# Kernel tuning notes

Measured on AMD Instinct MI355X. Metric: run time of the kernel, lower is better.

The kernel has to match this reference:

```python
import jax, jax.numpy as jnp
import numpy as np

B, S, HID = 2, 2048, 1024
NH, HD = 16, 64
EPS = 1e-12


def setup_inputs() -> dict:
    key = jax.random.key(0)
    ks = jax.random.split(key, 6)
    w_scale = 1.0 / np.sqrt(HID)
    return {
        "hidden_states": jax.random.normal(ks[0], (B, S, HID), dtype=jnp.float32),
        "attention_mask": jnp.ones((B, S), dtype=jnp.float32),
        "Wq": jax.random.normal(ks[1], (HID, HID), dtype=jnp.float32) * w_scale,
        "bq": jnp.zeros((HID,), dtype=jnp.float32),
        "Wk": jax.random.normal(ks[2], (HID, HID), dtype=jnp.float32) * w_scale,
        "bk": jnp.zeros((HID,), dtype=jnp.float32),
        "Wv": jax.random.normal(ks[3], (HID, HID), dtype=jnp.float32) * w_scale,
        "bv": jnp.zeros((HID,), dtype=jnp.float32),
        "Wd": jax.random.normal(ks[4], (HID, HID), dtype=jnp.float32) * w_scale,
        "bd": jnp.zeros((HID,), dtype=jnp.float32),
        "ln_gamma": jnp.ones((HID,), dtype=jnp.float32),
        "ln_beta": jnp.zeros((HID,), dtype=jnp.float32),
    }


def _heads(x):  # [B,S,HID] -> [B,NH,S,HD]
    return x.reshape(B, S, NH, HD).transpose(0, 2, 1, 3)


def reference(hidden_states, attention_mask, Wq, bq, Wk, bk, Wv, bv, Wd, bd, ln_gamma, ln_beta):
    # pre-LayerNorm
    mu = jnp.mean(hidden_states, axis=-1, keepdims=True)
    var = jnp.mean(jnp.square(hidden_states - mu), axis=-1, keepdims=True)
    h = (hidden_states - mu) * jax.lax.rsqrt(var + EPS) * ln_gamma + ln_beta

    q = _heads(h @ Wq.T + bq)  # [B,NH,S,HD]
    k = _heads(h @ Wk.T + bk)
    v = _heads(h @ Wv.T + bv)

    # additive mask: -1000 * (1 - mask), broadcast over heads and query pos
    add_mask = -1000.0 * (1.0 - attention_mask)[:, None, None, :]  # [B,1,1,S]

    # scale applied symmetrically to q and k: sqrt(sqrt(HD)) each
    scale = np.sqrt(np.sqrt(HD)).astype(np.float32)
    scores = jnp.einsum("bhqd,bhkd->bhqk", q / scale, k / scale) + add_mask
    probs = jax.nn.softmax(scores, axis=-1)  # dropout p=0 -> identity
    ctx = jnp.einsum("bhqk,bhkd->bhqd", probs, v)  # [B,NH,S,HD]

    ctx = ctx.transpose(0, 2, 1, 3).reshape(B, S, HID)
    return ctx @ Wd.T + bd
```

## Files before the change

### kernel.cpp

```cpp
#include <hip/hip_runtime.h>
#include <hip/hip_bf16.h>
#include <math.h>

#define BATCH 2
#define SEQ   2048
#define HID   1024
#define NH    16
#define HD    64
#define MROWS (BATCH * SEQ)
#define VSTR  4160

typedef unsigned short u16;
typedef short bf16x8 __attribute__((ext_vector_type(8)));
typedef short bf16x4 __attribute__((ext_vector_type(4)));
typedef float f32x4  __attribute__((ext_vector_type(4)));

#define LOG2E 1.4426950408889634f
#define C2    (0.125f * LOG2E)
#define M2F   23.083120f

static __device__ __forceinline__ u16 f2bf(float f) {
    union { float f; unsigned int u; } v; v.f = f;
    unsigned int r = (v.u + 0x7FFF + ((v.u >> 16) & 1)) >> 16;
    return (u16)r;
}

static __device__ __forceinline__ unsigned int pk_bf16(float a, float b) {
    union { __hip_bfloat162 h; unsigned int u; } r;
    float2 f; f.x = a; f.y = b;
    r.h = __float22bfloat162_rn(f);
    return r.u;
}

static __device__ __forceinline__ f32x4 mfma16(bf16x8 a, bf16x8 b, f32x4 c) {
    return __builtin_amdgcn_mfma_f32_16x16x32_bf16(a, b, c, 0, 0, 0);
}

static __device__ __forceinline__ f32x4 mfma16k16(bf16x4 a, bf16x4 b, f32x4 c) {
#if __has_builtin(__builtin_amdgcn_mfma_f32_16x16x16bf16_1k)
    return __builtin_amdgcn_mfma_f32_16x16x16bf16_1k(a, b, c, 0, 0, 0);
#else
    bf16x8 a8 = {a[0], a[1], a[2], a[3], 0, 0, 0, 0};
    bf16x8 b8 = {b[0], b[1], b[2], b[3], 0, 0, 0, 0};
    return __builtin_amdgcn_mfma_f32_16x16x32_bf16(a8, b8, c, 0, 0, 0);
#endif
}

static __device__ __forceinline__ void ldsload16(const void* g, void* l) {
    __builtin_amdgcn_global_load_lds(
        (const __attribute__((address_space(1))) void*)(unsigned long long)(uintptr_t)g,
        (__attribute__((address_space(3))) void*)(unsigned int)(uintptr_t)l,
        16, 0, 0);
}

__global__ __launch_bounds__(256) void prep_kernel(const float* __restrict__ x,
                                                   const float* __restrict__ gamma,
                                                   const float* __restrict__ beta,
                                                   u16* __restrict__ h,
                                                   const float* __restrict__ w0,
                                                   const float* __restrict__ w1,
                                                   const float* __restrict__ w2,
                                                   const float* __restrict__ w3,
                                                   u16* o0, u16* o1, u16* o2, u16* o3,
                                                   const float* __restrict__ maskg,
                                                   float* __restrict__ m2g)
{
    __shared__ float red[8];
    const int t = threadIdx.x;
    if (blockIdx.x >= 8192) {
        const int idx = ((blockIdx.x - 8192) * 256 + t) * 4;
        const float4 m = *(const float4*)(maskg + idx);
        float4 o;
        o.x = fmaf(-1000.0f * (1.0f - m.x), LOG2E, -M2F);
        o.y = fmaf(-1000.0f * (1.0f - m.y), LOG2E, -M2F);
        o.z = fmaf(-1000.0f * (1.0f - m.z), LOG2E, -M2F);
        o.w = fmaf(-1000.0f * (1.0f - m.w), LOG2E, -M2F);
        *(float4*)(m2g + idx) = o;
        return;
    }
    if (blockIdx.x < 4096) {
        const int blk = blockIdx.x;
        const int which = blk >> 10;
        const int lb = blk & 1023;
        const float* src = which == 0 ? w0 : which == 1 ? w1 : which == 2 ? w2 : w3;
        u16* dst = which == 0 ? o0 : which == 1 ? o1 : which == 2 ? o2 : o3;
        const int idx = (lb * 256 + t) * 4;
        const float4 f = *(const float4*)(src + idx);
        union { u16 s[4]; uint2 v; } p;
        p.s[0] = f2bf(f.x); p.s[1] = f2bf(f.y); p.s[2] = f2bf(f.z); p.s[3] = f2bf(f.w);
        *(uint2*)(dst + idx) = p.v;
        return;
    }
    const int row = blockIdx.x - 4096;
    const float4 xv = ((const float4*)(x + (size_t)row * HID))[t];
    float s  = xv.x + xv.y + xv.z + xv.w;
    float ss = xv.x * xv.x + xv.y * xv.y + xv.z * xv.z + xv.w * xv.w;
#pragma unroll
    for (int off = 32; off > 0; off >>= 1) {
        s  += __shfl_down(s, off);
        ss += __shfl_down(ss, off);
    }
    const int wid = t >> 6;
    if ((t & 63) == 0) { red[wid] = s; red[4 + wid] = ss; }
    __syncthreads();
    s  = red[0] + red[1] + red[2] + red[3];
    ss = red[4] + red[5] + red[6] + red[7];
    const float mu   = s * (1.0f / HID);
    const float var  = ss * (1.0f / HID) - mu * mu;
    const float rstd = rsqrtf(var + 1e-12f);
    const float4 g  = ((const float4*)gamma)[t];
    const float4 bb = ((const float4*)beta)[t];
    union { u16 s[4]; uint2 v; } p;
    p.s[0] = f2bf((xv.x - mu) * rstd * g.x + bb.x);
    p.s[1] = f2bf((xv.y - mu) * rstd * g.y + bb.y);
    p.s[2] = f2bf((xv.z - mu) * rstd * g.z + bb.z);
    p.s[3] = f2bf((xv.w - mu) * rstd * g.w + bb.w);
    ((uint2*)(h + (size_t)row * HID))[t] = p.v;
}

static __device__ __forceinline__ void gemm_core(const u16* __restrict__ A,
                                                 const u16* __restrict__ B,
                                                 int K, int bm, int bn,
                                                 u16* As, u16* Bs,
                                                 int wave, int lane,
                                                 f32x4 acc[4][4])
{
    const int l15  = lane & 15;
    const int quad = lane >> 4;
    const int wm = (wave >> 1) * 64;
    const int wn = (wave & 1) * 64;

    const int c1 = wave * 64 + lane;
    const int c2 = c1 + 256;
    const u16* A1 = A + (size_t)(bm + (c1 >> 2)) * K + (c1 & 3) * 8;
    const u16* A2 = A + (size_t)(bm + (c2 >> 2)) * K + (c2 & 3) * 8;
    const u16* B1 = B + (size_t)(bn + (c1 >> 2)) * K + (c1 & 3) * 8;
    const u16* B2 = B + (size_t)(bn + (c2 >> 2)) * K + (c2 & 3) * 8;
    const int o1 = wave * 512;
    const int o2 = 2048 + wave * 512;

    ldsload16(A1, As + o1);
    ldsload16(A2, As + o2);
    ldsload16(B1, Bs + o1);
    ldsload16(B2, Bs + o2);

    const int nstep = K >> 5;
    for (int i = 0; i < nstep; i++) {
        __syncthreads();
        const int cb = (i & 1) * 4096;
        if (i + 1 < nstep) {
            const int nb = ((i + 1) & 1) * 4096;
            const int k0 = (i + 1) * 32;
            ldsload16(A1 + k0, As + nb + o1);
            ldsload16(A2 + k0, As + nb + o2);
            ldsload16(B1 + k0, Bs + nb + o1);
            ldsload16(B2 + k0, Bs + nb + o2);
        }
        bf16x8 af[4], bfr[4];
#pragma unroll
        for (int mt = 0; mt < 4; mt++)
            af[mt] = *(const bf16x8*)&As[cb + (wm + mt * 16 + l15) * 32 + quad * 8];
#pragma unroll
        for (int nt = 0; nt < 4; nt++)
            bfr[nt] = *(const bf16x8*)&Bs[cb + (wn + nt * 16 + l15) * 32 + quad * 8];
#pragma unroll
        for (int mt = 0; mt < 4; mt++)
#pragma unroll
            for (int nt = 0; nt < 4; nt++)
                acc[mt][nt] = mfma16(af[mt], bfr[nt], acc[mt][nt]);
    }
}

__global__ __launch_bounds__(256) void qkv_gemm(const u16* __restrict__ h,
                                                const u16* __restrict__ wq,
                                                const u16* __restrict__ wk,
                                                const u16* __restrict__ wv,
                                                const float* __restrict__ bq,
                                                const float* __restrict__ bk,
                                                const float* __restrict__ bv,
                                                u16* __restrict__ qo,
                                                u16* __restrict__ ko,
                                                u16* __restrict__ vo)
{
    __shared__ __align__(16) u16 smemT[16384];
    u16* As = smemT;
    u16* Bs = smemT + 8192;
    const int blk  = blockIdx.x;
    const int t    = threadIdx.x;
    const int wave = t >> 6;
    const int lane = t & 63;
    const int l15  = lane & 15;
    const int quad = lane >> 4;
    const int wm = (wave >> 1) * 64;
    const int wn = (wave & 1) * 64;

    f32x4 acc[4][4];
#pragma unroll
    for (int mt = 0; mt < 4; mt++)
#pragma unroll
        for (int nt = 0; nt < 4; nt++) acc[mt][nt] = (f32x4)0.0f;

    if (blk < 512) {
        const u16* W     = (blk < 256) ? wq : wk;
        const float* bia = (blk < 256) ? bq : bk;
        u16* out         = (blk < 256) ? qo : ko;
        const int local = blk & 255;
        const int bm = (local >> 3) * 128;
        const int bn = (local & 7) * 128;
        gemm_core(h, W, HID, bm, bn, As, Bs, wave, lane, acc);

        float bv4[4];
#pragma unroll
        for (int nt = 0; nt < 4; nt++) bv4[nt] = bia[bn + wn + nt * 16 + l15];

        __syncthreads();
#pragma unroll
        for (int mt = 0; mt < 4; mt++)
#pragma unroll
            for (int r = 0; r < 4; r++) {
                const int row = wm + mt * 16 + quad * 4 + r;
#pragma unroll
                for (int nt = 0; nt < 4; nt++) {
                    const int colL = wn + nt * 16 + l15;
                    smemT[row * 128 + ((((colL >> 3) ^ (row & 7)) << 3) | (colL & 7))] =
                        f2bf(acc[mt][nt][r] + bv4[nt]);
                }
            }
        __syncthreads();
        {
            const int tr = t & 127;
            const int nh = t >> 7;
            const int m  = bm + tr;
            const int bI = m >> 11;
            const int sI = m & (SEQ - 1);
            const int n0 = bn + nh * 64;
            const int hhd = n0 >> 6;
            u16* dst = out + (((size_t)(bI * NH + hhd) * SEQ + sI) << 6);
#pragma unroll
            for (int j = 0; j < 8; j++) {
                const int colL = nh * 64 + j * 8;
                const uint4 v = *(const uint4*)&smemT[tr * 128 +
                    (((colL >> 3) ^ (tr & 7)) << 3)];
                *(uint4*)(dst + j * 8) = v;
            }
        }
    } else {
        const int local = blk - 512;
        const int bm = (local & 7) * 128;
        const int bn = (local >> 3) * 128;
        gemm_core(wv, h, HID, bm, bn, As, Bs, wave, lane, acc);

        __syncthreads();
#pragma unroll
        for (int mt = 0; mt < 4; mt++) {
            const f32x4 bm4 = *(const f32x4*)&bv[bm + wm + mt * 16 + quad * 4];
#pragma unroll
            for (int r = 0; r < 4; r++) {
                const int row = wm + mt * 16 + quad * 4 + r;
#pragma unroll
                for (int nt = 0; nt < 4; nt++) {
                    const int colL = wn + nt * 16 + l15;
                    smemT[row * 128 + ((((colL >> 3) ^ (row & 7)) << 3) | (colL & 7))] =
                        f2bf(acc[mt][nt][r] + bm4[r]);
                }
            }
        }
        __syncthreads();
        {
            const int fr = t & 127;
            const int th = t >> 7;
            u16* dst = vo + (size_t)(bm + fr) * VSTR + bn + th * 64;
#pragma unroll
            for (int j = 0; j < 8; j++) {
                const int colL = th * 64 + j * 8;
                const uint4 v = *(const uint4*)&smemT[fr * 128 +
                    (((colL >> 3) ^ (fr & 7)) << 3)];
                *(uint4*)(dst + j * 8) = v;
            }
        }
    }
}

__global__ __launch_bounds__(256) void out_gemm(const u16* __restrict__ ctx,
                                                const u16* __restrict__ wd,
                                                const float* __restrict__ bd,
                                                float* __restrict__ out)
{
    __shared__ u16 As[8192];
    __shared__ u16 Bs[8192];
    const int blk  = blockIdx.x;
    const int wave = threadIdx.x >> 6;
    const int lane = threadIdx.x & 63;
    const int l15  = lane & 15;
    const int quad = lane >> 4;
    const int wm = (wave >> 1) * 64;
    const int wn = (wave & 1) * 64;
    const int bm = (blk >> 3) * 128;
    const int bn = (blk & 7) * 128;

    f32x4 acc[4][4];
#pragma unroll
    for (int mt = 0; mt < 4; mt++)
#pragma unroll
        for (int nt = 0; nt < 4; nt++) acc[mt][nt] = (f32x4)0.0f;

    gemm_core(ctx, wd, HID, bm, bn, As, Bs, wave, lane, acc);

    float bv4[4];
#pragma unroll
    for (int nt = 0; nt < 4; nt++) bv4[nt] = bd[bn + wn + nt * 16 + l15];
#pragma unroll
    for (int mt = 0; mt < 4; mt++)
#pragma unroll
        for (int r = 0; r < 4; r++) {
            const int m = bm + wm + mt * 16 + quad * 4 + r;
#pragma unroll
            for (int nt = 0; nt < 4; nt++) {
                const int n = bn + wn + nt * 16 + l15;
                out[(size_t)m * HID + n] = acc[mt][nt][r] + bv4[nt];
            }
        }
}

__global__ __launch_bounds__(256) void attn_mfma(const u16* __restrict__ qb,
                                                 const u16* __restrict__ kb,
                                                 const u16* __restrict__ vtb,
                                                 const float* __restrict__ m2g,
                                                 u16* __restrict__ ctx)
{
    __shared__ __align__(16) char smem[32768];

    const int t    = threadIdx.x;
    const int wave = t >> 6;
    const int lane = t & 63;
    const int l15  = lane & 15;
    const int quad = lane >> 4;

    const int bh = blockIdx.x & 31;
    const int qt = blockIdx.x >> 5;
    const int b  = bh >> 4;
    const int hh = bh & 15;
    const int q0 = qt * 64;

    const size_t headoff = (size_t)(b * NH + hh) * SEQ * HD;
    const u16* kbase = kb + headoff;
    const u16* vbase = vtb + (size_t)(hh * HD) * VSTR + b * SEQ;
    const float* m2b = m2g + b * SEQ;

    bf16x8 Qf[2];
    {
        const int qrow = q0 + wave * 16 + l15;
#pragma unroll
        for (int ks2 = 0; ks2 < 2; ks2++)
            Qf[ks2] = *(const bf16x8*)(qb + headoff + (size_t)qrow * HD + ks2 * 32 + quad * 8);
    }

    f32x4 O[4];
#pragma unroll
    for (int mt2 = 0; mt2 < 4; mt2++) O[mt2] = (f32x4)0.0f;
    float ls = 0.0f;

    const int srow = lane >> 3;
    const int lcol = (lane & 7) ^ srow;
    const int swk0 = ((quad)     ^ (l15 & 7)) * 8;
    const int swk1 = ((quad + 4) ^ (l15 & 7)) * 8;
    const int g0 = wave * 2;

    ldsload16(kbase + (size_t)(g0 * 8 + srow) * HD + lcol * 8,           smem + g0 * 1024);
    ldsload16(kbase + (size_t)(g0 * 8 + 8 + srow) * HD + lcol * 8,       smem + g0 * 1024 + 1024);
    ldsload16(vbase + (size_t)(g0 * 8 + srow) * VSTR + lcol * 8,         smem + 16384 + g0 * 1024);
    ldsload16(vbase + (size_t)(g0 * 8 + 8 + srow) * VSTR + lcol * 8,     smem + 16384 + g0 * 1024 + 1024);

    for (int i = 0; i < 32; i++) {
        __syncthreads();
        const int c0 = i * 64;
        const u16* Ks  = (const u16*)(smem + (i & 1) * 8192);
        const u16* Vts = (const u16*)(smem + 16384 + (i & 1) * 8192);
        if (i + 1 < 32) {
            const int cn = c0 + 64;
            char* nbK = smem + ((i + 1) & 1) * 8192;
            char* nbV = smem + 16384 + ((i + 1) & 1) * 8192;
            ldsload16(kbase + (size_t)(cn + g0 * 8 + srow) * HD + lcol * 8,       nbK + g0 * 1024);
            ldsload16(kbase + (size_t)(cn + g0 * 8 + 8 + srow) * HD + lcol * 8,   nbK + g0 * 1024 + 1024);
            ldsload16(vbase + (size_t)(g0 * 8 + srow) * VSTR + cn + lcol * 8,     nbV + g0 * 1024);
            ldsload16(vbase + (size_t)(g0 * 8 + 8 + srow) * VSTR + cn + lcol * 8, nbV + g0 * 1024 + 1024);
        }

        bf16x4 Pk[4];
#pragma unroll
        for (int ks = 0; ks < 4; ks++) {
            const int rb = (ks * 16 + l15) * 64;
            const bf16x8 ka0 = *(const bf16x8*)&Ks[rb + swk0];
            const bf16x8 ka1 = *(const bf16x8*)&Ks[rb + swk1];
            f32x4 a = (f32x4)0.0f;
            a = mfma16(ka0, Qf[0], a);
            a = mfma16(ka1, Qf[1], a);
            const f32x4 mv = *(const f32x4*)(m2b + c0 + ks * 16 + quad * 4);
            const float p0 = __builtin_amdgcn_exp2f(fmaf(a[0], C2, mv[0]));
            const float p1 = __builtin_amdgcn_exp2f(fmaf(a[1], C2, mv[1]));
            const float p2 = __builtin_amdgcn_exp2f(fmaf(a[2], C2, mv[2]));
            const float p3 = __builtin_amdgcn_exp2f(fmaf(a[3], C2, mv[3]));
            ls += (p0 + p1) + (p2 + p3);
            union { unsigned int u[2]; bf16x4 v; } pk;
            pk.u[0] = pk_bf16(p0, p1);
            pk.u[1] = pk_bf16(p2, p3);
            Pk[ks] = pk.v;
        }

#pragma unroll
        for (int mt2 = 0; mt2 < 4; mt2++) {
            const u16* Vp = Vts + (mt2 * 16 + l15) * 64 + ((quad & 1) << 2);
            bf16x4 Va[4];
#pragma unroll
            for (int ks = 0; ks < 4; ks++)
                Va[ks] = *(const bf16x4*)(Vp +
                    ((((ks << 1) | (quad >> 1)) ^ (l15 & 7)) << 3));
            f32x4 acc = O[mt2];
#pragma unroll
            for (int ks = 0; ks < 4; ks++)
                acc = mfma16k16(Va[ks], Pk[ks], acc);
            O[mt2] = acc;
        }
    }

    ls += __shfl_xor(ls, 16);
    ls += __shfl_xor(ls, 32);
    const float linv = 1.0f / ls;

    __syncthreads();
    float* Ot = (float*)smem + wave * (16 * 68);
#pragma unroll
    for (int mt2 = 0; mt2 < 4; mt2++) {
        const f32x4 v = O[mt2] * linv;
        *(f32x4*)(Ot + l15 * 68 + mt2 * 16 + quad * 4) = v;
    }
    {
        const int ql  = lane >> 2;
        const int seg = lane & 3;
        const float* srcp = Ot + ql * 68 + seg * 16;
        u16* dstp = ctx + (size_t)(b * SEQ + q0 + wave * 16 + ql) * HID
                        + hh * 64 + seg * 16;
#pragma unroll
        for (int j = 0; j < 2; j++) {
            union { u16 s[8]; uint4 v; } p;
#pragma unroll
            for (int ii = 0; ii < 8; ii++) p.s[ii] = f2bf(srcp[j * 8 + ii]);
            *(uint4*)(dstp + j * 8) = p.v;
        }
    }
}

extern "C" void kernel_launch(void* const* d_in, const int* in_sizes, int n_in,
                              void* d_out, int out_size, void* d_ws, size_t ws_size,
                              hipStream_t stream)
{
    const float* hs    = (const float*)d_in[0];
    const float* mask  = (const float*)d_in[1];
    const float* Wq    = (const float*)d_in[2];
    const float* bq    = (const float*)d_in[3];
    const float* Wk    = (const float*)d_in[4];
    const float* bk    = (const float*)d_in[5];
    const float* Wv    = (const float*)d_in[6];
    const float* bv    = (const float*)d_in[7];
    const float* Wd    = (const float*)d_in[8];
    const float* bd    = (const float*)d_in[9];
    const float* gamma = (const float*)d_in[10];
    const float* beta  = (const float*)d_in[11];
    float* out = (float*)d_out;

    const size_t NE = (size_t)MROWS * HID;
    u16* ws   = (u16*)d_ws;
    u16* h    = ws;
    u16* qbb  = ws + NE;
    u16* kbb  = qbb + NE;
    u16* vtb  = kbb + NE;
    u16* ctxb = vtb + (size_t)HID * VSTR;
    u16* wqb  = ctxb + NE;
    u16* wkb  = wqb + HID * HID;
    u16* wvb  = wkb + HID * HID;
    u16* wdb  = wvb + HID * HID;
    float* m2 = (float*)(wdb + HID * HID);

    prep_kernel<<<8196, 256, 0, stream>>>(hs, gamma, beta, h,
                                          Wq, Wk, Wv, Wd, wqb, wkb, wvb, wdb,
                                          mask, m2);

    qkv_gemm<<<768, 256, 0, stream>>>(h, wqb, wkb, wvb, bq, bk, bv, qbb, kbb, vtb);

    attn_mfma<<<1024, 256, 0, stream>>>(qbb, kbb, vtb, m2, ctxb);

    out_gemm<<<256, 256, 0, stream>>>(ctxb, wdb, bd, out);
}
```

Baseline: 226.8 us.

## Split-K output GEMM with reduce kernel; register-staged padded K/V tiles in attention

The output projection is split into two K halves across 512 blocks. Each half writes partial sums, and a new reduce kernel adds them and applies the bias; the second partial reuses the dead h/q workspace region. This is meant to fill more CUs than the previous 256-block launch, at the cost of extra fp32 traffic and one more launch. Separately, the attention kernel now stages K/V tiles through registers into row-padded LDS buffers (stride 76) instead of async LDS loads with XOR swizzling, giving simpler addressing and a different global-load pattern.

```diff
diff --git a/kernel.cpp b/kernel.cpp
--- a/kernel.cpp
+++ b/kernel.cpp
@@ -9,6 +9,7 @@
 #define HD    64
 #define MROWS (BATCH * SEQ)
 #define VSTR  4160
+#define KROW  76
 
 typedef unsigned short u16;
 typedef short bf16x8 __attribute__((ext_vector_type(8)));
@@ -120,7 +121,7 @@
 
 static __device__ __forceinline__ void gemm_core(const u16* __restrict__ A,
                                                  const u16* __restrict__ B,
-                                                 int K, int bm, int bn,
+                                                 int ldk, int kspan, int bm, int bn,
                                                  u16* As, u16* Bs,
                                                  int wave, int lane,
                                                  f32x4 acc[4][4])
@@ -132,10 +133,10 @@
 
     const int c1 = wave * 64 + lane;
     const int c2 = c1 + 256;
-    const u16* A1 = A + (size_t)(bm + (c1 >> 2)) * K + (c1 & 3) * 8;
-    const u16* A2 = A + (size_t)(bm + (c2 >> 2)) * K + (c2 & 3) * 8;
-    const u16* B1 = B + (size_t)(bn + (c1 >> 2)) * K + (c1 & 3) * 8;
-    const u16* B2 = B + (size_t)(bn + (c2 >> 2)) * K + (c2 & 3) * 8;
+    const u16* A1 = A + (size_t)(bm + (c1 >> 2)) * ldk + (c1 & 3) * 8;
+    const u16* A2 = A + (size_t)(bm + (c2 >> 2)) * ldk + (c2 & 3) * 8;
+    const u16* B1 = B + (size_t)(bn + (c1 >> 2)) * ldk + (c1 & 3) * 8;
+    const u16* B2 = B + (size_t)(bn + (c2 >> 2)) * ldk + (c2 & 3) * 8;
     const int o1 = wave * 512;
     const int o2 = 2048 + wave * 512;
 
@@ -144,7 +145,7 @@
     ldsload16(B1, Bs + o1);
     ldsload16(B2, Bs + o2);
 
-    const int nstep = K >> 5;
+    const int nstep = kspan >> 5;
     for (int i = 0; i < nstep; i++) {
         __syncthreads();
         const int cb = (i & 1) * 4096;
@@ -207,7 +208,7 @@
         const int local = blk & 255;
         const int bm = (local >> 3) * 128;
         const int bn = (local & 7) * 128;
-        gemm_core(h, W, HID, bm, bn, As, Bs, wave, lane, acc);
+        gemm_core(h, W, HID, HID, bm, bn, As, Bs, wave, lane, acc);
 
         float bv4[4];
 #pragma unroll
@@ -248,7 +249,7 @@
         const int local = blk - 512;
         const int bm = (local & 7) * 128;
         const int bn = (local >> 3) * 128;
-        gemm_core(wv, h, HID, bm, bn, As, Bs, wave, lane, acc);
+        gemm_core(wv, h, HID, HID, bm, bn, As, Bs, wave, lane, acc);
 
         __syncthreads();
 #pragma unroll
@@ -281,22 +282,24 @@
     }
 }
 
-__global__ __launch_bounds__(256) void out_gemm(const u16* __restrict__ ctx,
-                                                const u16* __restrict__ wd,
-                                                const float* __restrict__ bd,
-                                                float* __restrict__ out)
+__global__ __launch_bounds__(256) void out_gemm_sk(const u16* __restrict__ ctx,
+                                                   const u16* __restrict__ wd,
+                                                   float* __restrict__ out0,
+                                                   float* __restrict__ outp1)
 {
     __shared__ u16 As[8192];
     __shared__ u16 Bs[8192];
     const int blk  = blockIdx.x;
+    const int ksel = blk >> 8;
+    const int local = blk & 255;
     const int wave = threadIdx.x >> 6;
     const int lane = threadIdx.x & 63;
     const int l15  = lane & 15;
     const int quad = lane >> 4;
     const int wm = (wave >> 1) * 64;
     const int wn = (wave & 1) * 64;
-    const int bm = (blk >> 3) * 128;
-    const int bn = (blk & 7) * 128;
+    const int bm = (local >> 3) * 128;
+    const int bn = (local & 7) * 128;
 
     f32x4 acc[4][4];
 #pragma unroll
@@ -304,11 +307,10 @@
 #pragma unroll
         for (int nt = 0; nt < 4; nt++) acc[mt][nt] = (f32x4)0.0f;
 
-    gemm_core(ctx, wd, HID, bm, bn, As, Bs, wave, lane, acc);
-
-    float bv4[4];
-#pragma unroll
-    for (int nt = 0; nt < 4; nt++) bv4[nt] = bd[bn + wn + nt * 16 + l15];
+    gemm_core(ctx + ksel * 512, wd + ksel * 512, HID, 512, bm, bn,
+              As, Bs, wave, lane, acc);
+
+    float* dstp = ksel ? outp1 : out0;
 #pragma unroll
     for (int mt = 0; mt < 4; mt++)
 #pragma unroll
@@ -317,9 +319,20 @@
 #pragma unroll
             for (int nt = 0; nt < 4; nt++) {
                 const int n = bn + wn + nt * 16 + l15;
-                out[(size_t)m * HID + n] = acc[mt][nt][r] + bv4[nt];
+                dstp[(size_t)m * HID + n] = acc[mt][nt][r];
             }
         }
+}
+
+__global__ __launch_bounds__(256) void reduce_out(const float* __restrict__ outp1,
+                                                  const float* __restrict__ bd,
+                                                  float* __restrict__ out)
+{
+    const int idx = (blockIdx.x * 256 + threadIdx.x) * 4;
+    const f32x4 a = *(const f32x4*)(out + idx);
+    const f32x4 b = *(const f32x4*)(outp1 + idx);
+    const f32x4 bias = *(const f32x4*)(bd + (idx & (HID - 1)));
+    *(f32x4*)(out + idx) = a + b + bias;
 }
 
 __global__ __launch_bounds__(256) void attn_mfma(const u16* __restrict__ qb,
@@ -328,7 +341,7 @@
                                                  const float* __restrict__ m2g,
                                                  u16* __restrict__ ctx)
 {
-    __shared__ __align__(16) char smem[32768];
+    __shared__ __align__(16) char smem[38912];
 
     const int t    = threadIdx.x;
     const int wave = t >> 6;
@@ -360,38 +373,44 @@
     for (int mt2 = 0; mt2 < 4; mt2++) O[mt2] = (f32x4)0.0f;
     float ls = 0.0f;
 
-    const int srow = lane >> 3;
-    const int lcol = (lane & 7) ^ srow;
-    const int swk0 = ((quad)     ^ (l15 & 7)) * 8;
-    const int swk1 = ((quad + 4) ^ (l15 & 7)) * 8;
-    const int g0 = wave * 2;
-
-    ldsload16(kbase + (size_t)(g0 * 8 + srow) * HD + lcol * 8,           smem + g0 * 1024);
-    ldsload16(kbase + (size_t)(g0 * 8 + 8 + srow) * HD + lcol * 8,       smem + g0 * 1024 + 1024);
-    ldsload16(vbase + (size_t)(g0 * 8 + srow) * VSTR + lcol * 8,         smem + 16384 + g0 * 1024);
-    ldsload16(vbase + (size_t)(g0 * 8 + 8 + srow) * VSTR + lcol * 8,     smem + 16384 + g0 * 1024 + 1024);
+    const int srow = t >> 2;
+    const int cp   = (t & 3) * 16;
+    const u16* kg0 = kbase + (size_t)srow * HD + cp;
+    const u16* vg0 = vbase + (size_t)srow * VSTR + cp;
+    const int woff = srow * KROW + cp;
+
+    uint4 kA = *(const uint4*)(kg0);
+    uint4 kB = *(const uint4*)(kg0 + 8);
+    uint4 vA = *(const uint4*)(vg0);
+    uint4 vB = *(const uint4*)(vg0 + 8);
 
     for (int i = 0; i < 32; i++) {
+        u16* Kb = (u16*)(smem + (i & 1) * 9728);
+        u16* Vb = (u16*)(smem + 19456 + (i & 1) * 9728);
+        *(uint4*)&Kb[woff]     = kA;
+        *(uint4*)&Kb[woff + 8] = kB;
+        *(uint4*)&Vb[woff]     = vA;
+        *(uint4*)&Vb[woff + 8] = vB;
+        if (i + 1 < 32) {
+            const u16* kg = kg0 + (size_t)(i + 1) * 64 * HD;
+            const u16* vg = vg0 + (i + 1) * 64;
+            kA = *(const uint4*)(kg);
+            kB = *(const uint4*)(kg + 8);
+            vA = *(const uint4*)(vg);
+            vB = *(const uint4*)(vg + 8);
+        }
         __syncthreads();
+
         const int c0 = i * 64;
-        const u16* Ks  = (const u16*)(smem + (i & 1) * 8192);
-        const u16* Vts = (const u16*)(smem + 16384 + (i & 1) * 8192);
-        if (i + 1 < 32) {
-            const int cn = c0 + 64;
-            char* nbK = smem + ((i + 1) & 1) * 8192;
-            char* nbV = smem + 16384 + ((i + 1) & 1) * 8192;
-            ldsload16(kbase + (size_t)(cn + g0 * 8 + srow) * HD + lcol * 8,       nbK + g0 * 1024);
-            ldsload16(kbase + (size_t)(cn + g0 * 8 + 8 + srow) * HD + lcol * 8,   nbK + g0 * 1024 + 1024);
-            ldsload16(vbase + (size_t)(g0 * 8 + srow) * VSTR + cn + lcol * 8,     nbV + g0 * 1024);
-            ldsload16(vbase + (size_t)(g0 * 8 + 8 + srow) * VSTR + cn + lcol * 8, nbV + g0 * 1024 + 1024);
-        }
+        const u16* Ks  = (const u16*)(smem + (i & 1) * 9728);
+        const u16* Vts = (const u16*)(smem + 19456 + (i & 1) * 9728);
 
         bf16x4 Pk[4];
 #pragma unroll
         for (int ks = 0; ks < 4; ks++) {
-            const int rb = (ks * 16 + l15) * 64;
-            const bf16x8 ka0 = *(const bf16x8*)&Ks[rb + swk0];
-            const bf16x8 ka1 = *(const bf16x8*)&Ks[rb + swk1];
+            const u16* Kp = Ks + (ks * 16 + l15) * KROW;
+            const bf16x8 ka0 = *(const bf16x8*)(Kp + quad * 8);
+            const bf16x8 ka1 = *(const bf16x8*)(Kp + 32 + quad * 8);
             f32x4 a = (f32x4)0.0f;
             a = mfma16(ka0, Qf[0], a);
             a = mfma16(ka1, Qf[1], a);
@@ -409,12 +428,11 @@
 
 #pragma unroll
         for (int mt2 = 0; mt2 < 4; mt2++) {
-            const u16* Vp = Vts + (mt2 * 16 + l15) * 64 + ((quad & 1) << 2);
+            const u16* Vp = Vts + (mt2 * 16 + l15) * KROW + quad * 4;
             bf16x4 Va[4];
 #pragma unroll
             for (int ks = 0; ks < 4; ks++)
-                Va[ks] = *(const bf16x4*)(Vp +
-                    ((((ks << 1) | (quad >> 1)) ^ (l15 & 7)) << 3));
+                Va[ks] = *(const bf16x4*)(Vp + ks * 16);
             f32x4 acc = O[mt2];
 #pragma unroll
             for (int ks = 0; ks < 4; ks++)
@@ -480,6 +498,7 @@
     u16* wvb  = wkb + HID * HID;
     u16* wdb  = wvb + HID * HID;
     float* m2 = (float*)(wdb + HID * HID);
+    float* outp1 = (float*)ws;
 
     prep_kernel<<<8196, 256, 0, stream>>>(hs, gamma, beta, h,
                                           Wq, Wk, Wv, Wd, wqb, wkb, wvb, wdb,
@@ -489,5 +508,6 @@
 
     attn_mfma<<<1024, 256, 0, stream>>>(qbb, kbb, vtb, m2, ctxb);
 
-    out_gemm<<<256, 256, 0, stream>>>(ctxb, wdb, bd, out);
-}
+    out_gemm_sk<<<512, 256, 0, stream>>>(ctxb, wdb, out, outp1);
+    reduce_out<<<4096, 256, 0, stream>>>(outp1, bd, out);
+}
```

After: 347.0 us. 1.53x slower.
